# Kernel tuning notes

Hardware: AMD Instinct MI355X
Metric: run time of the kernel (lower is better)

The kernel has to match this reference:

```python
import jax, jax.numpy as jnp
import numpy as np

S, N, D, F, L = 16, 64, 1270, 150, 8  # sentences, entities, emb dim, ffnn_size, num_labels


def _xavier(key, shape):
    lim = np.sqrt(6.0 / (shape[0] + shape[1])).astype(np.float32)
    return jax.random.uniform(key, shape, jnp.float32, -lim, lim)


def setup_inputs() -> dict:
    key = jax.random.key(0)
    ks = jax.random.split(key, 8)
    entity_emb = jax.random.normal(ks[0], (S, N, D), jnp.float32)
    entity_scores = jax.random.normal(ks[1], (S, N), jnp.float32)
    rel_labels = jax.random.randint(ks[2], (S, N, N), 0, L)
    num_predicted_entities = jax.random.randint(ks[3], (S,), 0, N)
    # Linear params stored [in, out] (y = x @ W + b), transpose of torch layout.
    W_in = _xavier(ks[4], (3 * D, F))
    b_in = jnp.zeros((F,), jnp.float32)
    W_h = _xavier(ks[5], (F, F))
    b_h = jnp.zeros((F,), jnp.float32)
    W_out = _xavier(ks[6], (F, L - 1))
    b_out = jnp.zeros((L - 1,), jnp.float32)
    return {
        "entity_emb": entity_emb,
        "entity_scores": entity_scores,
        "W_in": W_in, "b_in": b_in,
        "W_h": W_h, "b_h": b_h,
        "W_out": W_out, "b_out": b_out,
        "rel_labels": rel_labels,
        "num_predicted_entities": num_predicted_entities,
    }


def reference(entity_emb, entity_scores, W_in, b_in, W_h, b_h, W_out, b_out,
              rel_labels, num_predicted_entities):
    s, n, d = entity_emb.shape
    # pair_emb = concat([e1_tiled, e2_tiled, e1*e2]) @ W_in  ==  split-weight fused form
    # (avoids materializing the [S,N,N,3D] tensor; same math).
    W1, W2, W3 = W_in[:d], W_in[d:2 * d], W_in[2 * d:]
    h = (jnp.einsum('sid,df->sif', entity_emb, W1)[:, :, None, :]
         + jnp.einsum('sjd,df->sjf', entity_emb, W2)[:, None, :, :]
         + jnp.einsum('sid,sjd,df->sijf', entity_emb, entity_emb, W3)
         + b_in)  # [S,N,N,F]
    # NOTE: original applies two more Linear layers with NO nonlinearity between them.
    h = h @ W_h + b_h
    scores = h @ W_out + b_out  # [S,N,N,L-1]
    # dropout is identity at inference (reference baseline)
    rel = scores + entity_scores[:, :, None, None] + entity_scores[:, None, :, None]
    dummy = jnp.zeros((s, n, n, 1), rel.dtype)
    rel_scores = jnp.concatenate([dummy, rel], axis=3)  # [S,N,N,L]
    # per-element cross entropy (reduction='none'), then pair mask, then sum
    logp = jax.nn.log_softmax(rel_scores, axis=-1)
    ce = -jnp.take_along_axis(logp, rel_labels[..., None], axis=-1)[..., 0]  # [S,N,N]
    ent_mask = jnp.arange(n)[None, :] < num_predicted_entities[:, None]  # [S,N]
    pair_mask = ent_mask[:, :, None] & ent_mask[:, None, :]  # [S,N,N]
    loss = jnp.sum(jnp.where(pair_mask, ce, jnp.zeros((), ce.dtype)))
    return rel_scores, loss
```

## Files before the change

kernel.cpp:

```cpp
#include <hip/hip_runtime.h>
#include <hip/hip_bf16.h>
#include <stdint.h>

typedef __attribute__((ext_vector_type(8))) short bf16x8;
typedef __attribute__((ext_vector_type(16))) float f32x16;

#define S_ 16
#define N_ 64
#define D_ 1270
#define F_ 150
#define KP_ 1280
#define FP_ 160
#define NKT 80
#define LOSS_OFF (S_*N_*N_*8)

#define HSTR 172

__device__ inline short f2b(float x) {
    union { float f; uint32_t u; } v; v.f = x;
    uint32_t r = (v.u + 0x7fffu + ((v.u >> 16) & 1u)) >> 16;
    return (short)r;
}
__device__ inline bf16x8 as_bf16x8(uint4 u) {
    union { uint4 a; bf16x8 b; } c; c.a = u; return c.b;
}

__global__ void k_pack(const float* __restrict__ emb, const float* __restrict__ win,
                       const float* __restrict__ wh, const float* __restrict__ wout,
                       short* __restrict__ eapk, short* __restrict__ w3pk,
                       short* __restrict__ w12pk, short* __restrict__ whpk,
                       short* __restrict__ wopk) {
    int t = blockIdx.x * 256 + threadIdx.x;
    const int TOT_EA = S_ * NKT * 2 * 64;
    const int NW3 = NKT * 5 * 64, NW12 = NKT * 10 * 64, NWH = 10 * 5 * 64, NWO = 10 * 64;
    if (t < TOT_EA) {
        int l  = t & 63;
        int mt = (t >> 6) & 1;
        int kt = (t >> 7) % NKT;
        int s  = t / (NKT * 2 * 64);
        int i  = (l & 31) + mt * 32;
        int k0 = kt * 16 + (l >> 5) * 8;
        const float* src = emb + (size_t)(s * N_ + i) * D_;
        bf16x8 pk;
        if (k0 + 8 <= D_) {
            float2 v0 = *(const float2*)(src + k0);
            float2 v1 = *(const float2*)(src + k0 + 2);
            float2 v2 = *(const float2*)(src + k0 + 4);
            float2 v3 = *(const float2*)(src + k0 + 6);
            pk[0]=f2b(v0.x); pk[1]=f2b(v0.y); pk[2]=f2b(v1.x); pk[3]=f2b(v1.y);
            pk[4]=f2b(v2.x); pk[5]=f2b(v2.y); pk[6]=f2b(v3.x); pk[7]=f2b(v3.y);
        } else {
            #pragma unroll
            for (int u = 0; u < 8; ++u) {
                int k = k0 + u;
                pk[u] = (k < D_) ? f2b(src[k]) : (short)0;
            }
        }
        *(bf16x8*)(eapk + (size_t)t * 8) = pk;
        return;
    }
    int t0 = t - TOT_EA;
    if (t0 < NW3) {
        int l = t0 & 63, nt = (t0 >> 6) % 5, kt = t0 / 320;
        int k0 = kt * 16 + (l >> 5) * 8, f = (l & 31) + nt * 32;
        bf16x8 pk;
        #pragma unroll
        for (int u = 0; u < 8; ++u) {
            int k = k0 + u;
            pk[u] = (k < D_ && f < F_) ? f2b(win[((size_t)(2 * D_) + k) * F_ + f]) : (short)0;
        }
        *(bf16x8*)(w3pk + (size_t)t0 * 8) = pk;
    } else if (t0 < NW3 + NW12) {
        int t2 = t0 - NW3;
        int l = t2 & 63, nt = (t2 >> 6) % 10, kt = t2 / 640;
        int k0 = kt * 16 + (l >> 5) * 8, c = (l & 31) + nt * 32;
        bf16x8 pk;
        #pragma unroll
        for (int u = 0; u < 8; ++u) {
            int k = k0 + u;
            float val = 0.f;
            if (k < D_) {
                if (c < FP_) { if (c < F_) val = win[(size_t)k * F_ + c]; }
                else { int f = c - FP_; if (f < F_) val = win[((size_t)D_ + k) * F_ + f]; }
            }
            pk[u] = f2b(val);
        }
        *(bf16x8*)(w12pk + (size_t)t2 * 8) = pk;
    } else if (t0 < NW3 + NW12 + NWH) {
        int t3 = t0 - NW3 - NW12;
        int l = t3 & 63, nt = (t3 >> 6) % 5, kt = t3 / 320;
        int k0 = kt * 16 + (l >> 5) * 8, f = (l & 31) + nt * 32;
        bf16x8 pk;
        #pragma unroll
        for (int u = 0; u < 8; ++u) {
            int k = k0 + u;
            pk[u] = (k < F_ && f < F_) ? f2b(wh[(size_t)k * F_ + f]) : (short)0;
        }
        *(bf16x8*)(whpk + (size_t)t3 * 8) = pk;
    } else if (t0 < NW3 + NW12 + NWH + NWO) {
        int t4 = t0 - NW3 - NW12 - NWH;
        int l = t4 & 63, kt = t4 >> 6;
        int k0 = kt * 16 + (l >> 5) * 8, f = l & 31;
        bf16x8 pk;
        #pragma unroll
        for (int u = 0; u < 8; ++u) {
            int k = k0 + u;
            pk[u] = (k < F_ && f < 7) ? f2b(wout[k * 7 + f]) : (short)0;
        }
        *(bf16x8*)(wopk + (size_t)t4 * 8) = pk;
    }
}

__global__ __launch_bounds__(128) void k_p12(const short* __restrict__ eapk,
                                             const short* __restrict__ w12pk,
                                             const float* __restrict__ bin,
                                             float* __restrict__ p1, float* __restrict__ p2) {
    __shared__ float red[16][64];
    int bid = blockIdx.x;
    int x = bid & 7, k = bid >> 3;
    int s = x * 2 + (k / 20);
    int rr = k % 20;
    int nt = rr >> 1, mt = rr & 1;
    int lane = threadIdx.x & 63, ks = threadIdx.x >> 6;
    f32x16 acc;
    #pragma unroll
    for (int r = 0; r < 16; ++r) acc[r] = 0.f;
    const size_t abase = (size_t)s * NKT * 2 * 64 * 8;
    #pragma unroll 8
    for (int kt = ks * 40; kt < ks * 40 + 40; ++kt) {
        bf16x8 a = *(const bf16x8*)(eapk + abase + ((size_t)kt * 2 + mt) * 64 * 8 + (size_t)lane * 8);
        bf16x8 b = *(const bf16x8*)(w12pk + ((size_t)(kt * 10 + nt) * 64 + lane) * 8);
        acc = __builtin_amdgcn_mfma_f32_32x32x16_bf16(a, b, acc, 0, 0, 0);
    }
    if (ks == 1) {
        #pragma unroll
        for (int r = 0; r < 16; ++r) red[r][lane] = acc[r];
    }
    __syncthreads();
    if (ks == 0) {
        int c = (lane & 31) + nt * 32;
        #pragma unroll
        for (int r = 0; r < 16; ++r) {
            float v = acc[r] + red[r][lane];
            int i = (r & 3) + 8 * (r >> 2) + 4 * (lane >> 5) + mt * 32;
            if (c < FP_) {
                p1[(size_t)(s * N_ + i) * FP_ + c] = v;
            } else {
                int f = c - FP_;
                float bv = (f < F_) ? bin[f] : 0.f;
                p2[(size_t)(s * N_ + i) * FP_ + f] = v + bv;
            }
        }
    }
}

template<int NB>
__device__ __forceinline__ void run_gemm1(const char* ea, const char* w3,
                                          const float* ej0, const float* ej1,
                                          f32x16 (&acc)[2][3]) {
    uint4 euA, euB;
    uint4 bfA[3], bfB[3];

    auto fetch = [&](int kt, uint4& eu, uint4 (&bfv)[3]) {
        eu = *(const uint4*)(ea + (size_t)kt * 2048);
        #pragma unroll
        for (int nb = 0; nb < NB; ++nb)
            bfv[nb] = *(const uint4*)(w3 + (size_t)kt * 5120 + nb * 1024);
    };
    auto step = [&](int kt, const uint4& eu, const uint4 (&bfv)[3]) {
        float4 a0 = *(const float4*)(ej0 + kt * 16);
        float4 a1 = *(const float4*)(ej0 + kt * 16 + 4);
        float4 b0 = *(const float4*)(ej1 + kt * 16);
        float4 b1 = *(const float4*)(ej1 + kt * 16 + 4);
        float ev0[8] = {a0.x,a0.y,a0.z,a0.w,a1.x,a1.y,a1.z,a1.w};
        float ev1[8] = {b0.x,b0.y,b0.z,b0.w,b1.x,b1.y,b1.z,b1.w};
        uint32_t ew[4] = {eu.x, eu.y, eu.z, eu.w};
        union { uint32_t u[4]; bf16x8 v; } av0, av1;
        #pragma unroll
        for (int p = 0; p < 4; ++p) {
            float elo = __uint_as_float(ew[p] << 16);
            float ehi = __uint_as_float(ew[p] & 0xffff0000u);
            float f00 = elo * ev0[2*p], f01 = ehi * ev0[2*p+1];
            float f10 = elo * ev1[2*p], f11 = ehi * ev1[2*p+1];
            uint32_t p0, p1v;
            asm("v_cvt_pk_bf16_f32 %0, %1, %2" : "=v"(p0)  : "v"(f00), "v"(f01));
            asm("v_cvt_pk_bf16_f32 %0, %1, %2" : "=v"(p1v) : "v"(f10), "v"(f11));
            av0.u[p] = p0; av1.u[p] = p1v;
        }
        #pragma unroll
        for (int nb = 0; nb < NB; ++nb) {
            bf16x8 bb = as_bf16x8(bfv[nb]);
            acc[0][nb] = __builtin_amdgcn_mfma_f32_32x32x16_bf16(av0.v, bb, acc[0][nb], 0, 0, 0);
            acc[1][nb] = __builtin_amdgcn_mfma_f32_32x32x16_bf16(av1.v, bb, acc[1][nb], 0, 0, 0);
        }
    };

    fetch(0, euA, bfA);
    fetch(1, euB, bfB);
    #pragma unroll 1
    for (int kt = 0; kt < NKT; kt += 2) {
        step(kt, euA, bfA);
        if (kt + 2 < NKT) fetch(kt + 2, euA, bfA);
        step(kt + 1, euB, bfB);
        if (kt + 3 < NKT) fetch(kt + 3, euB, bfB);
    }
}

template<int NB, int NT0>
__device__ __forceinline__ void write_h(const f32x16 (&acc)[2][3], short* hB,
                                        const float* p1s, const float* p2r0,
                                        const float* p2r1, int lane, int mt) {
    #pragma unroll
    for (int nb = 0; nb < NB; ++nb) {
        const int f = (lane & 31) + (NT0 + nb) * 32;
        float p1v[16];
        #pragma unroll
        for (int r = 0; r < 16; ++r) {
            int i = (r & 3) + 8 * (r >> 2) + 4 * (lane >> 5) + mt * 32;
            p1v[r] = p1s[(size_t)i * FP_ + f];
        }
        const float p20 = p2r0[f], p21 = p2r1[f];
        #pragma unroll
        for (int r = 0; r < 16; ++r) {
            int i = (r & 3) + 8 * (r >> 2) + 4 * (lane >> 5) + mt * 32;
            hB[i * HSTR + f]             = f2b(acc[0][nb][r] + p1v[r] + p20);
            hB[64 * HSTR + i * HSTR + f] = f2b(acc[1][nb][r] + p1v[r] + p21);
        }
    }
}

__global__ __launch_bounds__(256, 1) void k_main(
    const float* __restrict__ emb, const float* __restrict__ esc,
    const short* __restrict__ eapk, const short* __restrict__ w3pk,
    const short* __restrict__ whpk, const short* __restrict__ wopk,
    const float* __restrict__ p1g, const float* __restrict__ p2g,
    const float* __restrict__ bhv, const float* __restrict__ bout,
    const int* __restrict__ labels, const int* __restrict__ nump,
    float* __restrict__ out) {

    __shared__ char lds[48128];
    float* sbuf = (float*)lds;
    float* ejB  = (float*)(lds + 4096);
    short* hB   = (short*)(lds + 4096);

    const int tid = threadIdx.x, lane = tid & 63, w = tid >> 6;
    const int mt = w & 1, nh = w >> 1;
    const int bid = blockIdx.x;
    const int x = bid & 7, kk = bid >> 3;
    const int s = x * 2 + (kk >> 5);
    const int j0 = (kk & 31) * 2;

    for (int idx = tid; idx < 2 * KP_; idx += 256) {
        int jr = idx / KP_, k = idx - jr * KP_;
        ejB[idx] = (k < D_) ? emb[(size_t)(s * N_ + j0 + jr) * D_ + k] : 0.f;
    }
    __syncthreads();

    f32x16 acc[2][3];
    #pragma unroll
    for (int jl = 0; jl < 2; ++jl)
        #pragma unroll
        for (int nb = 0; nb < 3; ++nb)
            #pragma unroll
            for (int r = 0; r < 16; ++r) acc[jl][nb][r] = 0.f;

    {
        const char* ea = (const char*)eapk + (size_t)s * 163840 + mt * 1024 + lane * 16;
        const char* w3 = (const char*)w3pk + (nh ? 3 : 0) * 1024 + lane * 16;
        const float* ej0 = ejB + ((lane >> 5) << 3);
        const float* ej1 = ej0 + KP_;
        if (nh == 0) run_gemm1<3>(ea, w3, ej0, ej1, acc);
        else         run_gemm1<2>(ea, w3, ej0, ej1, acc);
    }
    __syncthreads();

    {
        const float* p1s = p1g + (size_t)(s * N_) * FP_;
        const float* p2r0 = p2g + (size_t)(s * N_ + j0) * FP_;
        const float* p2r1 = p2r0 + FP_;
        if (nh == 0) write_h<3, 0>(acc, hB, p1s, p2r0, p2r1, lane, mt);
        else         write_h<2, 3>(acc, hB, p1s, p2r0, p2r1, lane, mt);
    }
    __syncthreads();

    f32x16 acc2[5];
    #pragma unroll
    for (int c = 0; c < 5; ++c)
        #pragma unroll
        for (int r = 0; r < 16; ++r) acc2[c][r] = 0.f;
    #pragma unroll 1
    for (int kt = 0; kt < 10; ++kt) {
        #pragma unroll
        for (int c = 0; c < 5; ++c) {
            int t = w + 4 * c;
            int jl2 = t / 10, tt = t % 10;
            int mt2 = tt / 5, nt2 = tt % 5;
            const short* ap = hB + jl2 * (64 * HSTR) + ((lane & 31) + mt2 * 32) * HSTR
                            + kt * 16 + ((lane >> 5) << 3);
            short4 alo = *(const short4*)ap;
            short4 ahi = *(const short4*)(ap + 4);
            union { short sh[8]; bf16x8 v; } av;
            av.sh[0] = alo.x; av.sh[1] = alo.y; av.sh[2] = alo.z; av.sh[3] = alo.w;
            av.sh[4] = ahi.x; av.sh[5] = ahi.y; av.sh[6] = ahi.z; av.sh[7] = ahi.w;
            bf16x8 b = *(const bf16x8*)(whpk + ((size_t)(kt * 5 + nt2) * 64 + lane) * 8);
            acc2[c] = __builtin_amdgcn_mfma_f32_32x32x16_bf16(av.v, b, acc2[c], 0, 0, 0);
        }
    }
    __syncthreads();

    #pragma unroll
    for (int c = 0; c < 5; ++c) {
        int t = w + 4 * c;
        int jl2 = t / 10, tt = t % 10;
        int mt2 = tt / 5, nt2 = tt % 5;
        int f = (lane & 31) + nt2 * 32;
        float bhf = (f < F_) ? bhv[f] : 0.f;
        #pragma unroll
        for (int r = 0; r < 16; ++r) {
            int i = (r & 3) + 8 * (r >> 2) + 4 * (lane >> 5) + mt2 * 32;
            short hv = (f < F_) ? f2b(acc2[c][r] + bhf) : (short)0;
            hB[jl2 * (64 * HSTR) + i * HSTR + f] = hv;
        }
    }
    __syncthreads();

    {
        int jl3 = w >> 1, mt3 = w & 1;
        f32x16 acc3;
        #pragma unroll
        for (int r = 0; r < 16; ++r) acc3[r] = 0.f;
        #pragma unroll 1
        for (int kt = 0; kt < 10; ++kt) {
            const short* ap = hB + jl3 * (64 * HSTR) + ((lane & 31) + mt3 * 32) * HSTR
                            + kt * 16 + ((lane >> 5) << 3);
            short4 alo = *(const short4*)ap;
            short4 ahi = *(const short4*)(ap + 4);
            union { short sh[8]; bf16x8 v; } av;
            av.sh[0] = alo.x; av.sh[1] = alo.y; av.sh[2] = alo.z; av.sh[3] = alo.w;
            av.sh[4] = ahi.x; av.sh[5] = ahi.y; av.sh[6] = ahi.z; av.sh[7] = ahi.w;
            bf16x8 b = *(const bf16x8*)(wopk + ((size_t)(kt * 64) + lane) * 8);
            acc3 = __builtin_amdgcn_mfma_f32_32x32x16_bf16(av.v, b, acc3, 0, 0, 0);
        }
        int c3 = lane & 31;
        if (c3 < 7) {
            float bo = bout[c3];
            #pragma unroll
            for (int r = 0; r < 16; ++r) {
                int i = (r & 3) + 8 * (r >> 2) + 4 * (lane >> 5) + mt3 * 32;
                sbuf[jl3 * 512 + i * 8 + c3] = acc3[r] + bo;
            }
        }
    }
    __syncthreads();

    if (tid < 128) {
        int jl = tid >> 6;
        int i = tid & 63;
        int j = j0 + jl;
        const float esi = esc[s * N_ + i];
        const float esj = esc[s * N_ + j];
        float rr[8];
        rr[0] = 0.f;
        #pragma unroll
        for (int l = 1; l < 8; ++l) rr[l] = sbuf[jl * 512 + i * 8 + (l - 1)] + esi + esj;

        float4* op = (float4*)(out + ((size_t)(s * N_ + i) * N_ + j) * 8);
        op[0] = make_float4(rr[0], rr[1], rr[2], rr[3]);
        op[1] = make_float4(rr[4], rr[5], rr[6], rr[7]);

        float m = rr[0];
        #pragma unroll
        for (int l = 1; l < 8; ++l) m = fmaxf(m, rr[l]);
        float sum = 0.f;
        #pragma unroll
        for (int l = 0; l < 8; ++l) sum += expf(rr[l] - m);
        const float lse = m + logf(sum);

        const int lab = labels[(s * N_ + i) * N_ + j];
        float ce = lse - rr[lab];
        const int np = nump[s];
        float v = (i < np && j < np) ? ce : 0.f;
        #pragma unroll
        for (int off = 32; off; off >>= 1) v += __shfl_down(v, off);
        if ((tid & 63) == 0) atomicAdd(out + LOSS_OFF, v);
    }
}

extern "C" void kernel_launch(void* const* d_in, const int* in_sizes, int n_in,
                              void* d_out, int out_size, void* d_ws, size_t ws_size,
                              hipStream_t stream) {
    const float* emb    = (const float*)d_in[0];
    const float* esc    = (const float*)d_in[1];
    const float* Win    = (const float*)d_in[2];
    const float* bin    = (const float*)d_in[3];
    const float* Wh     = (const float*)d_in[4];
    const float* bh     = (const float*)d_in[5];
    const float* Wout   = (const float*)d_in[6];
    const float* bout   = (const float*)d_in[7];
    const int*   labels = (const int*)d_in[8];
    const int*   nump   = (const int*)d_in[9];
    float* out = (float*)d_out;

    char* ws = (char*)d_ws;
    short* eapk  = (short*)(ws);
    short* w3pk  = (short*)(ws + 2621440);
    short* w12pk = (short*)(ws + 3031040);
    short* whpk  = (short*)(ws + 3850240);
    short* wopk  = (short*)(ws + 3901440);
    float* p1    = (float*)(ws + 3911680);
    float* p2    = (float*)(ws + 4567040);

    hipMemsetAsync(out + LOSS_OFF, 0, sizeof(float), stream);

    const int TOT_EA = S_ * NKT * 2 * 64;
    const int NW = NKT * 5 * 64 + NKT * 10 * 64 + 10 * 5 * 64 + 10 * 64;
    k_pack<<<(TOT_EA + NW + 255) / 256, 256, 0, stream>>>(emb, Win, Wh, Wout,
                                                          eapk, w3pk, w12pk, whpk, wopk);
    k_p12<<<320, 128, 0, stream>>>(eapk, w12pk, bin, p1, p2);
    k_main<<<S_ * 32, 256, 0, stream>>>(emb, esc, eapk, w3pk, whpk, wopk, p1, p2,
                                        bh, bout, labels, nump, out);
}
```

Before: 90.10 us.

## Stage GEMM1 operands into LDS with double-buffered async global_load_lds

Replaces the per-wave register-prefetched global loads of packed embedding and W3 fragments with a block-cooperative, double-buffered LDS staging pipeline using global_load_lds, four k-tiles per stage. Each wave now reads fragments from LDS, so the W3 tile loads once per block instead of once per wave. The ej rows are read directly from global memory rather than copied into LDS first, with special handling for the padded last k-tile. This adds a barrier per stage and raises LDS use to 56KB.

```diff
diff --git a/kernel.cpp b/kernel.cpp
--- a/kernel.cpp
+++ b/kernel.cpp
@@ -9,20 +9,17 @@
 #define N_ 64
 #define D_ 1270
 #define F_ 150
-#define KP_ 1280
 #define FP_ 160
 #define NKT 80
 #define LOSS_OFF (S_*N_*N_*8)
 
 #define HSTR 172
+#define STGB 28672
 
 __device__ inline short f2b(float x) {
     union { float f; uint32_t u; } v; v.f = x;
     uint32_t r = (v.u + 0x7fffu + ((v.u >> 16) & 1u)) >> 16;
     return (short)r;
-}
-__device__ inline bf16x8 as_bf16x8(uint4 u) {
-    union { uint4 a; bf16x8 b; } c; c.a = u; return c.b;
 }
 
 __global__ void k_pack(const float* __restrict__ emb, const float* __restrict__ win,
@@ -154,55 +151,45 @@
     }
 }
 
-template<int NB>
-__device__ __forceinline__ void run_gemm1(const char* ea, const char* w3,
-                                          const float* ej0, const float* ej1,
-                                          f32x16 (&acc)[2][3]) {
-    uint4 euA, euB;
-    uint4 bfA[3], bfB[3];
-
-    auto fetch = [&](int kt, uint4& eu, uint4 (&bfv)[3]) {
-        eu = *(const uint4*)(ea + (size_t)kt * 2048);
-        #pragma unroll
-        for (int nb = 0; nb < NB; ++nb)
-            bfv[nb] = *(const uint4*)(w3 + (size_t)kt * 5120 + nb * 1024);
-    };
-    auto step = [&](int kt, const uint4& eu, const uint4 (&bfv)[3]) {
-        float4 a0 = *(const float4*)(ej0 + kt * 16);
-        float4 a1 = *(const float4*)(ej0 + kt * 16 + 4);
-        float4 b0 = *(const float4*)(ej1 + kt * 16);
-        float4 b1 = *(const float4*)(ej1 + kt * 16 + 4);
-        float ev0[8] = {a0.x,a0.y,a0.z,a0.w,a1.x,a1.y,a1.z,a1.w};
-        float ev1[8] = {b0.x,b0.y,b0.z,b0.w,b1.x,b1.y,b1.z,b1.w};
-        uint32_t ew[4] = {eu.x, eu.y, eu.z, eu.w};
-        union { uint32_t u[4]; bf16x8 v; } av0, av1;
-        #pragma unroll
-        for (int p = 0; p < 4; ++p) {
-            float elo = __uint_as_float(ew[p] << 16);
-            float ehi = __uint_as_float(ew[p] & 0xffff0000u);
-            float f00 = elo * ev0[2*p], f01 = ehi * ev0[2*p+1];
-            float f10 = elo * ev1[2*p], f11 = ehi * ev1[2*p+1];
-            uint32_t p0, p1v;
-            asm("v_cvt_pk_bf16_f32 %0, %1, %2" : "=v"(p0)  : "v"(f00), "v"(f01));
-            asm("v_cvt_pk_bf16_f32 %0, %1, %2" : "=v"(p1v) : "v"(f10), "v"(f11));
-            av0.u[p] = p0; av1.u[p] = p1v;
-        }
-        #pragma unroll
-        for (int nb = 0; nb < NB; ++nb) {
-            bf16x8 bb = as_bf16x8(bfv[nb]);
-            acc[0][nb] = __builtin_amdgcn_mfma_f32_32x32x16_bf16(av0.v, bb, acc[0][nb], 0, 0, 0);
-            acc[1][nb] = __builtin_amdgcn_mfma_f32_32x32x16_bf16(av1.v, bb, acc[1][nb], 0, 0, 0);
-        }
-    };
-
-    fetch(0, euA, bfA);
-    fetch(1, euB, bfB);
-    #pragma unroll 1
-    for (int kt = 0; kt < NKT; kt += 2) {
-        step(kt, euA, bfA);
-        if (kt + 2 < NKT) fetch(kt + 2, euA, bfA);
-        step(kt + 1, euB, bfB);
-        if (kt + 3 < NKT) fetch(kt + 3, euB, bfB);
+__device__ __forceinline__ void stage_ss(const char* ea, const char* w3,
+                                         char* dst, int w, int lane) {
+    #pragma unroll
+    for (int q = 0; q < 7; ++q) {
+        const int n = w + 4 * q;
+        const char* src = (n < 8) ? (ea + (n << 10)) : (w3 + ((n - 8) << 10));
+        __builtin_amdgcn_global_load_lds(
+            (const __attribute__((address_space(1))) void*)(src + (lane << 4)),
+            (__attribute__((address_space(3))) void*)(dst + (n << 10) + (lane << 4)),
+            16, 0, 0);
+    }
+}
+
+template<int NB, int NT0>
+__device__ __forceinline__ void g1_step(const char* bb, int kk, int mt, int lane,
+                                        const float4& e0a, const float4& e0b,
+                                        const float4& e1a, const float4& e1b,
+                                        f32x16 (&acc)[2][3]) {
+    uint4 eu = *(const uint4*)(bb + kk * 2048 + mt * 1024 + (lane << 4));
+    float ev0[8] = {e0a.x,e0a.y,e0a.z,e0a.w,e0b.x,e0b.y,e0b.z,e0b.w};
+    float ev1[8] = {e1a.x,e1a.y,e1a.z,e1a.w,e1b.x,e1b.y,e1b.z,e1b.w};
+    uint32_t ew[4] = {eu.x, eu.y, eu.z, eu.w};
+    union { uint32_t u[4]; bf16x8 v; } av0, av1;
+    #pragma unroll
+    for (int p = 0; p < 4; ++p) {
+        float elo = __uint_as_float(ew[p] << 16);
+        float ehi = __uint_as_float(ew[p] & 0xffff0000u);
+        float f00 = elo * ev0[2*p], f01 = ehi * ev0[2*p+1];
+        float f10 = elo * ev1[2*p], f11 = ehi * ev1[2*p+1];
+        uint32_t p0, p1v;
+        asm("v_cvt_pk_bf16_f32 %0, %1, %2" : "=v"(p0)  : "v"(f00), "v"(f01));
+        asm("v_cvt_pk_bf16_f32 %0, %1, %2" : "=v"(p1v) : "v"(f10), "v"(f11));
+        av0.u[p] = p0; av1.u[p] = p1v;
+    }
+    #pragma unroll
+    for (int nb = 0; nb < NB; ++nb) {
+        bf16x8 b8 = *(const bf16x8*)(bb + 8192 + kk * 5120 + (NT0 + nb) * 1024 + (lane << 4));
+        acc[0][nb] = __builtin_amdgcn_mfma_f32_32x32x16_bf16(av0.v, b8, acc[0][nb], 0, 0, 0);
+        acc[1][nb] = __builtin_amdgcn_mfma_f32_32x32x16_bf16(av1.v, b8, acc[1][nb], 0, 0, 0);
     }
 }
 
@@ -238,23 +225,23 @@
     const int* __restrict__ labels, const int* __restrict__ nump,
     float* __restrict__ out) {
 
-    __shared__ char lds[48128];
-    float* sbuf = (float*)lds;
-    float* ejB  = (float*)(lds + 4096);
-    short* hB   = (short*)(lds + 4096);
+    __shared__ char lds[57344];
+    short* hB   = (short*)lds;
+    float* sbuf = (float*)(lds + 44032);
 
     const int tid = threadIdx.x, lane = tid & 63, w = tid >> 6;
     const int mt = w & 1, nh = w >> 1;
+    const int hi8 = (lane >> 5) << 3;
     const int bid = blockIdx.x;
-    const int x = bid & 7, kk = bid >> 3;
-    const int s = x * 2 + (kk >> 5);
-    const int j0 = (kk & 31) * 2;
-
-    for (int idx = tid; idx < 2 * KP_; idx += 256) {
-        int jr = idx / KP_, k = idx - jr * KP_;
-        ejB[idx] = (k < D_) ? emb[(size_t)(s * N_ + j0 + jr) * D_ + k] : 0.f;
-    }
-    __syncthreads();
+    const int x = bid & 7, kk2 = bid >> 3;
+    const int s = x * 2 + (kk2 >> 5);
+    const int j0 = (kk2 & 31) * 2;
+
+    const char* easrc = (const char*)eapk + (size_t)s * 163840;
+    const char* w3src = (const char*)w3pk;
+    const float* ejp0 = emb + (size_t)(s * N_ + j0) * D_;
+    const float* ejp1 = ejp0 + D_;
+    char* stg = lds;
 
     f32x16 acc[2][3];
     #pragma unroll
@@ -264,15 +251,44 @@
             #pragma unroll
             for (int r = 0; r < 16; ++r) acc[jl][nb][r] = 0.f;
 
-    {
-        const char* ea = (const char*)eapk + (size_t)s * 163840 + mt * 1024 + lane * 16;
-        const char* w3 = (const char*)w3pk + (nh ? 3 : 0) * 1024 + lane * 16;
-        const float* ej0 = ejB + ((lane >> 5) << 3);
-        const float* ej1 = ej0 + KP_;
-        if (nh == 0) run_gemm1<3>(ea, w3, ej0, ej1, acc);
-        else         run_gemm1<2>(ea, w3, ej0, ej1, acc);
-    }
-    __syncthreads();
+    stage_ss(easrc, w3src, stg, w, lane);
+    __syncthreads();
+
+    #pragma unroll 1
+    for (int ss = 0; ss < 20; ++ss) {
+        const int cur = ss & 1;
+        if (ss < 19)
+            stage_ss(easrc + (size_t)(ss + 1) * 8192,
+                     w3src + (size_t)(ss + 1) * 20480,
+                     stg + (cur ^ 1) * STGB, w, lane);
+        const char* bb = stg + cur * STGB;
+        #pragma unroll
+        for (int kk = 0; kk < 4; ++kk) {
+            const int kt = ss * 4 + kk;
+            float4 e0a, e0b, e1a, e1b;
+            if (kt != 79) {
+                const int a0 = kt * 16 + hi8;
+                e0a = *(const float4*)(ejp0 + a0);
+                e0b = *(const float4*)(ejp0 + a0 + 4);
+                e1a = *(const float4*)(ejp1 + a0);
+                e1b = *(const float4*)(ejp1 + a0 + 4);
+            } else {
+                e0a = make_float4(0.f, 0.f, 0.f, 0.f);
+                e0b = e0a; e1a = e0a; e1b = e0a;
+                if (hi8 == 0) {
+                    e0a = *(const float4*)(ejp0 + 1264);
+                    e1a = *(const float4*)(ejp1 + 1264);
+                    float2 t0 = *(const float2*)(ejp0 + 1268);
+                    float2 t1 = *(const float2*)(ejp1 + 1268);
+                    e0b.x = t0.x; e0b.y = t0.y;
+                    e1b.x = t1.x; e1b.y = t1.y;
+                }
+            }
+            if (nh == 0) g1_step<3, 0>(bb, kk, mt, lane, e0a, e0b, e1a, e1b, acc);
+            else         g1_step<2, 3>(bb, kk, mt, lane, e0a, e0b, e1a, e1b, acc);
+        }
+        __syncthreads();
+    }
 
     {
         const float* p1s = p1g + (size_t)(s * N_) * FP_;
@@ -296,7 +312,7 @@
             int jl2 = t / 10, tt = t % 10;
             int mt2 = tt / 5, nt2 = tt % 5;
             const short* ap = hB + jl2 * (64 * HSTR) + ((lane & 31) + mt2 * 32) * HSTR
-                            + kt * 16 + ((lane >> 5) << 3);
+                            + kt * 16 + hi8;
             short4 alo = *(const short4*)ap;
             short4 ahi = *(const short4*)(ap + 4);
             union { short sh[8]; bf16x8 v; } av;
@@ -332,7 +348,7 @@
         #pragma unroll 1
         for (int kt = 0; kt < 10; ++kt) {
             const short* ap = hB + jl3 * (64 * HSTR) + ((lane & 31) + mt3 * 32) * HSTR
-                            + kt * 16 + ((lane >> 5) << 3);
+                            + kt * 16 + hi8;
             short4 alo = *(const short4*)ap;
             short4 ahi = *(const short4*)(ap + 4);
             union { short sh[8]; bf16x8 v; } av;
```

Measured after the change: 94.45 us. +4.8%, slower.
